# Kernel tuning notes

Hardware: AMD Instinct MI355X
Metric: run time of the kernel (lower is better)

Reference implementation:

```python
import jax, jax.numpy as jnp
import numpy as np

B, N, F, E, D = 2, 50000, 128, 800000, 4


def setup_inputs() -> dict:
    key = jax.random.key(0)
    ks = jax.random.split(key, 6)
    X = jax.random.normal(ks[0], (B, N, F), dtype=jnp.float32)
    u_val = jax.random.normal(ks[1], (E, D), dtype=jnp.float32)
    u_rows = jax.random.randint(ks[2], (E,), 0, N, dtype=jnp.int32)
    u_cols = jax.random.randint(ks[3], (E,), 0, N, dtype=jnp.int32)
    mu = jax.random.uniform(ks[4], (1, D), minval=-0.05, maxval=0.05, dtype=jnp.float32)
    # sigma kept away from 0 so sigma^2 in the denominator is numerically sane
    sigma = jax.random.uniform(ks[5], (1, D), minval=0.5, maxval=1.5, dtype=jnp.float32)
    return {"X": X, "u_val": u_val, "u_rows": u_rows, "u_cols": u_cols,
            "mu": mu, "sigma": sigma, "u_shape": N}


def reference(X, u_val, u_rows, u_cols, mu, sigma, u_shape):
    n = u_shape  # python int, static
    # per-edge Gaussian kernel log-weight: -0.5 * sum_d (u-mu)^2 / (sigma^2+eps)
    w = -0.5 * jnp.sum(jnp.square(u_val - mu) / (jnp.square(sigma) + 1e-14), axis=1)  # [E]
    # sparse (segment) softmax over rows == tf.sparse.softmax on reordered SparseTensor
    m = jax.ops.segment_max(w, u_rows, num_segments=n)          # [N]
    e = jnp.exp(w - m[u_rows])                                  # [E]
    s = jax.ops.segment_sum(e, u_rows, num_segments=n)          # [N]
    sm = e / s[u_rows]                                          # [E]
    # sparse-dense matmul: D[b,i,f] = sum_{edges e: row=i} sm_e * X[b, col_e, f]
    Xt = jnp.transpose(X, (1, 0, 2))                            # [N,B,F]
    msg = sm[:, None, None] * Xt[u_cols]                        # [E,B,F]
    Dn = jax.ops.segment_sum(msg, u_rows, num_segments=n)       # [N,B,F]
    return jnp.transpose(Dn, (1, 0, 2))                         # [B,N,F]
```

## Files before the change

kernel.cpp:

```cpp
#include <hip/hip_runtime.h>

constexpr int Bc = 2;
constexpr int Fc = 128;
constexpr int F4 = Fc / 4;
constexpr int ROWS_PER_BLOCK = 4;
constexpr int EPT = 8;
constexpr int BIN_EDGES = 256 * EPT;

typedef float vfloat4 __attribute__((ext_vector_type(4)));

__device__ __forceinline__ unsigned short f2bf(float f) {
    unsigned u = __float_as_uint(f);
    unsigned r = (u + 0x7FFFu + ((u >> 16) & 1u)) >> 16;
    return (unsigned short)r;
}
__device__ __forceinline__ float bf2f(unsigned short h) {
    return __uint_as_float(((unsigned)h) << 16);
}

__device__ __forceinline__ void nt_store4(float4 v, float4* p) {
    vfloat4 q = {v.x, v.y, v.z, v.w};
    __builtin_nontemporal_store(q, (vfloat4*)p);
}

__global__ void conv_kernel(const float4* __restrict__ X4, ushort4* __restrict__ Xb, int N) {
    int t = blockIdx.x * 256 + threadIdx.x;
    if (t >= N * F4) return;
    int b  = blockIdx.y;
    int n  = t >> 5;
    int f4 = t & 31;
    float4 v = X4[(size_t)b * N * F4 + t];
    ushort4 o;
    o.x = f2bf(v.x); o.y = f2bf(v.y); o.z = f2bf(v.z); o.w = f2bf(v.w);
    Xb[(size_t)n * (Bc * F4) + b * F4 + f4] = o;
}

__global__ void init_cursor(int* __restrict__ bucket_cursor, int cap, int nbuk) {
    int t = threadIdx.x;
    if (t < nbuk) bucket_cursor[t] = t * cap;
}

__global__ __launch_bounds__(256) void bin_kernel(const float4* __restrict__ uval,
                                                  const float* __restrict__ mu,
                                                  const float* __restrict__ sigma,
                                                  const int* __restrict__ rows,
                                                  const int* __restrict__ cols,
                                                  int2* __restrict__ bucket_buf,
                                                  int* __restrict__ bucket_cursor,
                                                  int E, int cap, int nbuk) {
    __shared__ int hist[256];
    __shared__ int excl[256];
    __shared__ int fill[256];
    __shared__ int chunkb[256];
    __shared__ int sh[256];
    __shared__ int2 staged[BIN_EDGES];

    int t = threadIdx.x;
    hist[t] = 0;

    float m0 = mu[0], m1 = mu[1], m2 = mu[2], m3 = mu[3];
    float i0 = 1.0f / (sigma[0] * sigma[0] + 1e-14f);
    float i1 = 1.0f / (sigma[1] * sigma[1] + 1e-14f);
    float i2 = 1.0f / (sigma[2] * sigma[2] + 1e-14f);
    float i3 = 1.0f / (sigma[3] * sigma[3] + 1e-14f);
    __syncthreads();

    int e0 = blockIdx.x * BIN_EDGES;
    int meta_r[EPT];
    float ev_r[EPT];
    int buk_r[EPT];
    #pragma unroll
    for (int it = 0; it < EPT; ++it) {
        int e = e0 + it * 256 + t;
        if (e < E) {
            int r = rows[e];
            int c = cols[e];
            float4 u = uval[e];
            float d0 = u.x - m0, d1 = u.y - m1, d2 = u.z - m2, d3 = u.w - m3;
            float w = -0.5f * (d0 * d0 * i0 + d1 * d1 * i1 + d2 * d2 * i2 + d3 * d3 * i3);
            ev_r[it]   = expf(w);
            meta_r[it] = (r << 16) | c;
            buk_r[it]  = r >> 8;
            atomicAdd(&hist[buk_r[it]], 1);
        } else {
            buk_r[it] = -1;
        }
    }
    __syncthreads();

    int v = hist[t];
    sh[t] = v;
    __syncthreads();
    for (int off = 1; off < 256; off <<= 1) {
        int a = (t >= off) ? sh[t - off] : 0;
        __syncthreads();
        sh[t] += a;
        __syncthreads();
    }
    excl[t] = sh[t] - v;

    if (t < nbuk && v > 0) chunkb[t] = atomicAdd(&bucket_cursor[t], v);
    fill[t] = sh[t] - v;
    __syncthreads();

    #pragma unroll
    for (int it = 0; it < EPT; ++it) {
        if (buk_r[it] >= 0) {
            int rk = atomicAdd(&fill[buk_r[it]], 1);
            staged[rk] = make_int2(meta_r[it], __float_as_int(ev_r[it]));
        }
    }
    __syncthreads();

    int nst = min(BIN_EDGES, E - e0);
    for (int k = t; k < nst; k += 256) {
        int2 x = staged[k];
        int buk = ((unsigned)x.x) >> 24;
        int dest = chunkb[buk] + (k - excl[buk]);
        if (dest < (buk + 1) * cap)
            bucket_buf[dest] = x;
    }
}

__global__ void bucket_scan(const int* __restrict__ bucket_cursor,
                            int* __restrict__ csr_base, int cap, int nbuk) {
    __shared__ int sh[256];
    int t = threadIdx.x;
    int sz = (t < nbuk) ? (bucket_cursor[t] - t * cap) : 0;
    sh[t] = sz;
    __syncthreads();
    for (int off = 1; off < 256; off <<= 1) {
        int a = (t >= off) ? sh[t - off] : 0;
        __syncthreads();
        sh[t] += a;
        __syncthreads();
    }
    csr_base[t] = sh[t] - sz;
    if (t == nbuk - 1) csr_base[nbuk] = sh[t];
}

__global__ __launch_bounds__(256) void csr_kernel(const int2* __restrict__ bucket_buf,
                                                  const int* __restrict__ bucket_cursor,
                                                  const int* __restrict__ csr_base,
                                                  int2* __restrict__ pairs,
                                                  int* __restrict__ rowstart,
                                                  int cap, int N, int E) {
    __shared__ int hist[256];
    __shared__ int excl[256];
    __shared__ int cur[256];
    __shared__ int sh[256];
    int b = blockIdx.x;
    int t = threadIdx.x;
    int base  = b * cap;
    int size  = min(bucket_cursor[b] - base, cap);
    int cbase = csr_base[b];
    hist[t] = 0;
    __syncthreads();
    for (int k = t; k < size; k += 256) {
        unsigned m = (unsigned)bucket_buf[base + k].x;
        atomicAdd(&hist[(m >> 16) & 0xFF], 1);
    }
    __syncthreads();
    int v = hist[t];
    sh[t] = v;
    __syncthreads();
    for (int off = 1; off < 256; off <<= 1) {
        int a = (t >= off) ? sh[t - off] : 0;
        __syncthreads();
        sh[t] += a;
        __syncthreads();
    }
    excl[t] = sh[t] - v;
    cur[t]  = sh[t] - v;
    int row = b * 256 + t;
    if (row < N) rowstart[row] = cbase + excl[t];
    if (b == 0 && t == 0) rowstart[N] = E;
    __syncthreads();
    for (int k = t; k < size; k += 256) {
        int2 x = bucket_buf[base + k];
        unsigned m = (unsigned)x.x;
        int rk = atomicAdd(&cur[(m >> 16) & 0xFF], 1);
        pairs[cbase + rk] = make_int2((int)(m & 0xFFFFu), x.y);
    }
}

__global__ __launch_bounds__(256) void spmm_bf16(const ushort4* __restrict__ Xb,
                                                 const int2* __restrict__ pairs,
                                                 const int* __restrict__ rowstart,
                                                 float4* __restrict__ out4, int N) {
    int lane = threadIdx.x & 63;
    int i = blockIdx.x * ROWS_PER_BLOCK + (threadIdx.x >> 6);
    if (i >= N) return;
    int start = rowstart[i];
    int end   = rowstart[i + 1];
    float4 acc = {0.f, 0.f, 0.f, 0.f};
    float sum = 0.f;
    if (start < end) {
        int j = start;
        for (; j + 1 < end; j += 2) {
            int2 p0 = pairs[j];
            int2 p1 = pairs[j + 1];
            ushort4 x0 = Xb[(size_t)p0.x * 64 + lane];
            ushort4 x1 = Xb[(size_t)p1.x * 64 + lane];
            float e0 = __int_as_float(p0.y);
            float e1 = __int_as_float(p1.y);
            sum += e0 + e1;
            acc.x = fmaf(e0, bf2f(x0.x), acc.x);
            acc.y = fmaf(e0, bf2f(x0.y), acc.y);
            acc.z = fmaf(e0, bf2f(x0.z), acc.z);
            acc.w = fmaf(e0, bf2f(x0.w), acc.w);
            acc.x = fmaf(e1, bf2f(x1.x), acc.x);
            acc.y = fmaf(e1, bf2f(x1.y), acc.y);
            acc.z = fmaf(e1, bf2f(x1.z), acc.z);
            acc.w = fmaf(e1, bf2f(x1.w), acc.w);
        }
        if (j < end) {
            int2 p0 = pairs[j];
            ushort4 x0 = Xb[(size_t)p0.x * 64 + lane];
            float e0 = __int_as_float(p0.y);
            sum += e0;
            acc.x = fmaf(e0, bf2f(x0.x), acc.x);
            acc.y = fmaf(e0, bf2f(x0.y), acc.y);
            acc.z = fmaf(e0, bf2f(x0.z), acc.z);
            acc.w = fmaf(e0, bf2f(x0.w), acc.w);
        }
        float inv = 1.0f / sum;
        acc.x *= inv; acc.y *= inv; acc.z *= inv; acc.w *= inv;
    }
    int b  = lane >> 5;
    int f4 = lane & 31;
    nt_store4(acc, &out4[(size_t)b * N * F4 + (size_t)i * F4 + f4]);
}

__global__ __launch_bounds__(256) void spmm_f32(const float4* __restrict__ X4,
                                                const int2* __restrict__ pairs,
                                                const int* __restrict__ rowstart,
                                                float4* __restrict__ out4, int N) {
    int lane = threadIdx.x & 63;
    int i = blockIdx.x * ROWS_PER_BLOCK + (threadIdx.x >> 6);
    if (i >= N) return;
    int start = rowstart[i];
    int end   = rowstart[i + 1];
    int b  = lane >> 5;
    int f4 = lane & 31;
    float4 acc = {0.f, 0.f, 0.f, 0.f};
    float sum = 0.f;
    if (start < end) {
        int xbase = b * N * F4 + f4;
        for (int j = start; j < end; ++j) {
            int2 p = pairs[j];
            float ev = __int_as_float(p.y);
            sum += ev;
            float4 x = X4[xbase + (size_t)p.x * F4];
            acc.x = fmaf(ev, x.x, acc.x);
            acc.y = fmaf(ev, x.y, acc.y);
            acc.z = fmaf(ev, x.z, acc.z);
            acc.w = fmaf(ev, x.w, acc.w);
        }
        float inv = 1.0f / sum;
        acc.x *= inv; acc.y *= inv; acc.z *= inv; acc.w *= inv;
    }
    nt_store4(acc, &out4[(size_t)b * N * F4 + (size_t)i * F4 + f4]);
}

extern "C" void kernel_launch(void* const* d_in, const int* in_sizes, int n_in,
                              void* d_out, int out_size, void* d_ws, size_t ws_size,
                              hipStream_t stream) {
    const float* X      = (const float*)d_in[0];
    const float* u_val  = (const float*)d_in[1];
    const int*   u_rows = (const int*)d_in[2];
    const int*   u_cols = (const int*)d_in[3];
    const float* mu     = (const float*)d_in[4];
    const float* sigma  = (const float*)d_in[5];

    const int E = in_sizes[2];
    const int N = in_sizes[0] / (Bc * Fc);
    const int nbuk = (N + 255) >> 8;

    size_t off = 0;
    auto carve = [&](size_t bytes) -> char* {
        char* p = (char*)d_ws + off;
        off = (off + bytes + 255) & ~(size_t)255;
        return p;
    };
    int*  bucket_cursor = (int*)carve(256 * 4);
    int*  csr_base      = (int*)carve(257 * 4);
    int*  rowstart      = (int*)carve((size_t)(N + 1) * 4);
    int2* pairs         = (int2*)carve((size_t)E * 8);

    size_t xb_bytes = (size_t)N * Bc * Fc * 2;
    size_t avail    = (ws_size > off) ? (ws_size - off) : 0;
    int cap = 6144;
    size_t buck_bytes = (size_t)nbuk * cap * 8;
    if (buck_bytes + 512 > avail) {
        cap = (int)((avail - 512) / ((size_t)nbuk * 8));
        buck_bytes = (size_t)nbuk * cap * 8;
    }
    int2* bucket_buf = (int2*)carve(buck_bytes);
    bool use_bf16 = (off + xb_bytes) <= ws_size;
    ushort4* Xb = use_bf16 ? (ushort4*)carve(xb_bytes) : nullptr;

    init_cursor<<<1, 256, 0, stream>>>(bucket_cursor, cap, nbuk);
    if (use_bf16) {
        dim3 cgrid((N * F4 + 255) / 256, Bc);
        conv_kernel<<<cgrid, 256, 0, stream>>>((const float4*)X, Xb, N);
    }
    bin_kernel<<<(E + BIN_EDGES - 1) / BIN_EDGES, 256, 0, stream>>>(
        (const float4*)u_val, mu, sigma, u_rows, u_cols,
        bucket_buf, bucket_cursor, E, cap, nbuk);
    bucket_scan<<<1, 256, 0, stream>>>(bucket_cursor, csr_base, cap, nbuk);
    csr_kernel<<<nbuk, 256, 0, stream>>>(bucket_buf, bucket_cursor, csr_base,
                                         pairs, rowstart, cap, N, E);
    if (use_bf16) {
        spmm_bf16<<<(N + ROWS_PER_BLOCK - 1) / ROWS_PER_BLOCK, 256, 0, stream>>>(
            Xb, pairs, rowstart, (float4*)d_out, N);
    } else {
        spmm_f32<<<(N + ROWS_PER_BLOCK - 1) / ROWS_PER_BLOCK, 256, 0, stream>>>(
            (const float4*)X, pairs, rowstart, (float4*)d_out, N);
    }
}
```

Baseline: 116.3 us.

## Fuse bf16 conversion into binning kernel, fold bucket scan, batch spmm gathers

Merges the X-to-bf16 conversion blocks into the edge binning launch, replaces the init kernel with a memset, and moves the bucket prefix scan into each csr block so two small launches disappear. Bucket cursors now count relative offsets, and the final rowstart is taken from the scanned sum. The spmm loop loads up to 64 (col, weight) pairs per wave cooperatively, broadcasts them with shuffles and issues 8 independent gathers at a time. The aim is fewer launches and more memory-level parallelism in the gather, at the cost of redundant scans in every csr block and more registers in spmm.

```diff
diff --git a/kernel.cpp b/kernel.cpp
--- a/kernel.cpp
+++ b/kernel.cpp
@@ -17,37 +17,22 @@
 __device__ __forceinline__ float bf2f(unsigned short h) {
     return __uint_as_float(((unsigned)h) << 16);
 }
-
 __device__ __forceinline__ void nt_store4(float4 v, float4* p) {
     vfloat4 q = {v.x, v.y, v.z, v.w};
     __builtin_nontemporal_store(q, (vfloat4*)p);
 }
 
-__global__ void conv_kernel(const float4* __restrict__ X4, ushort4* __restrict__ Xb, int N) {
-    int t = blockIdx.x * 256 + threadIdx.x;
-    if (t >= N * F4) return;
-    int b  = blockIdx.y;
-    int n  = t >> 5;
-    int f4 = t & 31;
-    float4 v = X4[(size_t)b * N * F4 + t];
-    ushort4 o;
-    o.x = f2bf(v.x); o.y = f2bf(v.y); o.z = f2bf(v.z); o.w = f2bf(v.w);
-    Xb[(size_t)n * (Bc * F4) + b * F4 + f4] = o;
-}
-
-__global__ void init_cursor(int* __restrict__ bucket_cursor, int cap, int nbuk) {
-    int t = threadIdx.x;
-    if (t < nbuk) bucket_cursor[t] = t * cap;
-}
-
-__global__ __launch_bounds__(256) void bin_kernel(const float4* __restrict__ uval,
-                                                  const float* __restrict__ mu,
-                                                  const float* __restrict__ sigma,
-                                                  const int* __restrict__ rows,
-                                                  const int* __restrict__ cols,
-                                                  int2* __restrict__ bucket_buf,
-                                                  int* __restrict__ bucket_cursor,
-                                                  int E, int cap, int nbuk) {
+__global__ __launch_bounds__(256) void prep_kernel(const float4* __restrict__ uval,
+                                                   const float* __restrict__ mu,
+                                                   const float* __restrict__ sigma,
+                                                   const int* __restrict__ rows,
+                                                   const int* __restrict__ cols,
+                                                   int2* __restrict__ bucket_buf,
+                                                   int* __restrict__ bucket_cursor,
+                                                   const float4* __restrict__ X4,
+                                                   ushort4* __restrict__ Xb,
+                                                   int E, int N, int cap, int nbuk,
+                                                   int nbin) {
     __shared__ int hist[256];
     __shared__ int excl[256];
     __shared__ int fill[256];
@@ -56,8 +41,24 @@
     __shared__ int2 staged[BIN_EDGES];
 
     int t = threadIdx.x;
+
+    if (blockIdx.x >= nbin) {
+        long idx = (long)(blockIdx.x - nbin) * 256 + t;
+        long tot = (long)Bc * N * F4;
+        if (idx < tot) {
+            int b  = (int)(idx / ((long)N * F4));
+            int nt_ = (int)(idx - (long)b * N * F4);
+            int n  = nt_ >> 5;
+            int f4 = nt_ & 31;
+            float4 v = X4[(size_t)b * N * F4 + nt_];
+            ushort4 o;
+            o.x = f2bf(v.x); o.y = f2bf(v.y); o.z = f2bf(v.z); o.w = f2bf(v.w);
+            Xb[(size_t)n * (Bc * F4) + b * F4 + f4] = o;
+        }
+        return;
+    }
+
     hist[t] = 0;
-
     float m0 = mu[0], m1 = mu[1], m2 = mu[2], m3 = mu[3];
     float i0 = 1.0f / (sigma[0] * sigma[0] + 1e-14f);
     float i1 = 1.0f / (sigma[1] * sigma[1] + 1e-14f);
@@ -98,9 +99,9 @@
         __syncthreads();
     }
     excl[t] = sh[t] - v;
+    fill[t] = sh[t] - v;
 
     if (t < nbuk && v > 0) chunkb[t] = atomicAdd(&bucket_cursor[t], v);
-    fill[t] = sh[t] - v;
     __syncthreads();
 
     #pragma unroll
@@ -116,46 +117,41 @@
     for (int k = t; k < nst; k += 256) {
         int2 x = staged[k];
         int buk = ((unsigned)x.x) >> 24;
-        int dest = chunkb[buk] + (k - excl[buk]);
-        if (dest < (buk + 1) * cap)
-            bucket_buf[dest] = x;
-    }
-}
-
-__global__ void bucket_scan(const int* __restrict__ bucket_cursor,
-                            int* __restrict__ csr_base, int cap, int nbuk) {
-    __shared__ int sh[256];
-    int t = threadIdx.x;
-    int sz = (t < nbuk) ? (bucket_cursor[t] - t * cap) : 0;
-    sh[t] = sz;
-    __syncthreads();
-    for (int off = 1; off < 256; off <<= 1) {
-        int a = (t >= off) ? sh[t - off] : 0;
-        __syncthreads();
-        sh[t] += a;
-        __syncthreads();
-    }
-    csr_base[t] = sh[t] - sz;
-    if (t == nbuk - 1) csr_base[nbuk] = sh[t];
+        int rel = chunkb[buk] + (k - excl[buk]);
+        if (rel < cap)
+            bucket_buf[(size_t)buk * cap + rel] = x;
+    }
 }
 
 __global__ __launch_bounds__(256) void csr_kernel(const int2* __restrict__ bucket_buf,
                                                   const int* __restrict__ bucket_cursor,
-                                                  const int* __restrict__ csr_base,
                                                   int2* __restrict__ pairs,
                                                   int* __restrict__ rowstart,
-                                                  int cap, int N, int E) {
+                                                  int cap, int N, int nbuk) {
     __shared__ int hist[256];
     __shared__ int excl[256];
     __shared__ int cur[256];
     __shared__ int sh[256];
     int b = blockIdx.x;
     int t = threadIdx.x;
-    int base  = b * cap;
-    int size  = min(bucket_cursor[b] - base, cap);
-    int cbase = csr_base[b];
+
+    int szt = (t < nbuk) ? min(bucket_cursor[t], cap) : 0;
+    sh[t] = szt;
+    __syncthreads();
+    for (int off = 1; off < 256; off <<= 1) {
+        int a = (t >= off) ? sh[t - off] : 0;
+        __syncthreads();
+        sh[t] += a;
+        __syncthreads();
+    }
+    int cbase = (b == 0) ? 0 : sh[b - 1];
+    int size  = min(bucket_cursor[b], cap);
+    if (b == nbuk - 1 && t == 0) rowstart[N] = sh[nbuk - 1];
+    __syncthreads();
+
     hist[t] = 0;
     __syncthreads();
+    int base = b * cap;
     for (int k = t; k < size; k += 256) {
         unsigned m = (unsigned)bucket_buf[base + k].x;
         atomicAdd(&hist[(m >> 16) & 0xFF], 1);
@@ -174,7 +170,6 @@
     cur[t]  = sh[t] - v;
     int row = b * 256 + t;
     if (row < N) rowstart[row] = cbase + excl[t];
-    if (b == 0 && t == 0) rowstart[N] = E;
     __syncthreads();
     for (int k = t; k < size; k += 256) {
         int2 x = bucket_buf[base + k];
@@ -193,37 +188,37 @@
     if (i >= N) return;
     int start = rowstart[i];
     int end   = rowstart[i + 1];
+    int len   = end - start;
     float4 acc = {0.f, 0.f, 0.f, 0.f};
     float sum = 0.f;
-    if (start < end) {
-        int j = start;
-        for (; j + 1 < end; j += 2) {
-            int2 p0 = pairs[j];
-            int2 p1 = pairs[j + 1];
-            ushort4 x0 = Xb[(size_t)p0.x * 64 + lane];
-            ushort4 x1 = Xb[(size_t)p1.x * 64 + lane];
-            float e0 = __int_as_float(p0.y);
-            float e1 = __int_as_float(p1.y);
-            sum += e0 + e1;
-            acc.x = fmaf(e0, bf2f(x0.x), acc.x);
-            acc.y = fmaf(e0, bf2f(x0.y), acc.y);
-            acc.z = fmaf(e0, bf2f(x0.z), acc.z);
-            acc.w = fmaf(e0, bf2f(x0.w), acc.w);
-            acc.x = fmaf(e1, bf2f(x1.x), acc.x);
-            acc.y = fmaf(e1, bf2f(x1.y), acc.y);
-            acc.z = fmaf(e1, bf2f(x1.z), acc.z);
-            acc.w = fmaf(e1, bf2f(x1.w), acc.w);
-        }
-        if (j < end) {
-            int2 p0 = pairs[j];
-            ushort4 x0 = Xb[(size_t)p0.x * 64 + lane];
-            float e0 = __int_as_float(p0.y);
-            sum += e0;
-            acc.x = fmaf(e0, bf2f(x0.x), acc.x);
-            acc.y = fmaf(e0, bf2f(x0.y), acc.y);
-            acc.z = fmaf(e0, bf2f(x0.z), acc.z);
-            acc.w = fmaf(e0, bf2f(x0.w), acc.w);
-        }
+    for (int c = 0; c < len; c += 64) {
+        int m = min(64, len - c);
+        int2 myp = make_int2(0, 0);
+        if (lane < m) myp = pairs[start + c + lane];
+        for (int g = 0; g < m; g += 8) {
+            int   colv[8];
+            float evv[8];
+            #pragma unroll
+            for (int e = 0; e < 8; ++e) {
+                colv[e] = __shfl(myp.x, g + e);
+                evv[e]  = __int_as_float(__shfl(myp.y, g + e));
+            }
+            ushort4 xs[8];
+            #pragma unroll
+            for (int e = 0; e < 8; ++e)
+                xs[e] = Xb[(size_t)colv[e] * 64 + lane];
+            #pragma unroll
+            for (int e = 0; e < 8; ++e) {
+                float ev = evv[e];
+                sum += ev;
+                acc.x = fmaf(ev, bf2f(xs[e].x), acc.x);
+                acc.y = fmaf(ev, bf2f(xs[e].y), acc.y);
+                acc.z = fmaf(ev, bf2f(xs[e].z), acc.z);
+                acc.w = fmaf(ev, bf2f(xs[e].w), acc.w);
+            }
+        }
+    }
+    if (len > 0) {
         float inv = 1.0f / sum;
         acc.x *= inv; acc.y *= inv; acc.z *= inv; acc.w *= inv;
     }
@@ -284,7 +279,6 @@
         return p;
     };
     int*  bucket_cursor = (int*)carve(256 * 4);
-    int*  csr_base      = (int*)carve(257 * 4);
     int*  rowstart      = (int*)carve((size_t)(N + 1) * 4);
     int2* pairs         = (int2*)carve((size_t)E * 8);
 
@@ -300,17 +294,16 @@
     bool use_bf16 = (off + xb_bytes) <= ws_size;
     ushort4* Xb = use_bf16 ? (ushort4*)carve(xb_bytes) : nullptr;
 
-    init_cursor<<<1, 256, 0, stream>>>(bucket_cursor, cap, nbuk);
-    if (use_bf16) {
-        dim3 cgrid((N * F4 + 255) / 256, Bc);
-        conv_kernel<<<cgrid, 256, 0, stream>>>((const float4*)X, Xb, N);
-    }
-    bin_kernel<<<(E + BIN_EDGES - 1) / BIN_EDGES, 256, 0, stream>>>(
+    hipMemsetAsync(bucket_cursor, 0, 256 * 4, stream);
+
+    const int nbin  = (E + BIN_EDGES - 1) / BIN_EDGES;
+    const int nconv = use_bf16 ? (int)(((long)Bc * N * F4 + 255) / 256) : 0;
+    prep_kernel<<<nbin + nconv, 256, 0, stream>>>(
         (const float4*)u_val, mu, sigma, u_rows, u_cols,
-        bucket_buf, bucket_cursor, E, cap, nbuk);
-    bucket_scan<<<1, 256, 0, stream>>>(bucket_cursor, csr_base, cap, nbuk);
-    csr_kernel<<<nbuk, 256, 0, stream>>>(bucket_buf, bucket_cursor, csr_base,
-                                         pairs, rowstart, cap, N, E);
+        bucket_buf, bucket_cursor, (const float4*)X, Xb,
+        E, N, cap, nbuk, nbin);
+    csr_kernel<<<nbuk, 256, 0, stream>>>(bucket_buf, bucket_cursor,
+                                         pairs, rowstart, cap, N, nbuk);
     if (use_bf16) {
         spmm_bf16<<<(N + ROWS_PER_BLOCK - 1) / ROWS_PER_BLOCK, 256, 0, stream>>>(
             Xb, pairs, rowstart, (float4*)d_out, N);
```

New measurement: 100.1 us. -13.9%, faster.
